# Kernel tuning notes

Measured on AMD Instinct MI355X. Metric: run time of the kernel, lower is better.

## Reference

```python
import jax, jax.numpy as jnp
import numpy as np

N_NODES = 250
IN_F = 18
OUT_F = 48
NEG_SLOPE = 0.2
EPS = 1e-16


def gat_conv(x, edge_index, w_gat, att_src, att_dst, b_gat):
    # PyG GATConv, heads=1, concat=True, add_self_loops=True
    n = x.shape[0]
    h = x @ w_gat.T                      # [N, OUT_F]
    loop = jnp.arange(n)
    src = jnp.concatenate([edge_index[0], loop])
    dst = jnp.concatenate([edge_index[1], loop])
    a_s = h @ att_src                    # [N]
    a_d = h @ att_dst                    # [N]
    e = jax.nn.leaky_relu(a_s[src] + a_d[dst], NEG_SLOPE)  # [E+N]
    m = jax.ops.segment_max(e, dst, num_segments=n)
    ex = jnp.exp(e - m[dst])
    denom = jax.ops.segment_sum(ex, dst, num_segments=n)
    alpha = ex / (denom[dst] + EPS)
    out = jax.ops.segment_sum(alpha[:, None] * h[src], dst, num_segments=n)
    return out + b_gat


def setup_inputs() -> dict:
    key = jax.random.key(0)
    ks = jax.random.split(key, 24)

    def lin(kw, kb, out_d, in_d):
        s = 1.0 / np.sqrt(in_d)
        W = jax.random.uniform(kw, (out_d, in_d), minval=-s, maxval=s, dtype=jnp.float32)
        b = jax.random.uniform(kb, (out_d,), minval=-s, maxval=s, dtype=jnp.float32)
        return W, b

    x = jax.random.normal(ks[0], (N_NODES, IN_F), dtype=jnp.float32)
    edge_index = jax.random.randint(ks[1], (2, 4000), 0, N_NODES)
    edge_weight = jax.random.uniform(ks[2], (4000,), dtype=jnp.float32)
    residue_onehot = jax.random.uniform(ks[3], (8,), dtype=jnp.float32)
    pssm = jax.random.normal(ks[4], (20,), dtype=jnp.float32)

    w_gat = jax.random.normal(ks[5], (OUT_F, IN_F), dtype=jnp.float32) * (1.0 / np.sqrt(IN_F))
    att_src = jax.random.normal(ks[6], (OUT_F,), dtype=jnp.float32) * 0.1
    att_dst = jax.random.normal(ks[7], (OUT_F,), dtype=jnp.float32) * 0.1
    b_gat = jnp.zeros((OUT_F,), dtype=jnp.float32)

    W0, b0 = lin(ks[8], ks[9], 4000, 12000)
    W1, b1 = lin(ks[10], ks[11], 800, 4028)
    W2, b2 = lin(ks[12], ks[13], 400, 800)
    W3, b3 = lin(ks[14], ks[15], 200, 400)
    W4, b4 = lin(ks[16], ks[17], 1, 200)

    return dict(x=x, edge_index=edge_index, edge_weight=edge_weight,
                residue_onehot=residue_onehot, pssm=pssm,
                w_gat=w_gat, att_src=att_src, att_dst=att_dst, b_gat=b_gat,
                W0=W0, b0=b0, W1=W1, b1=b1, W2=W2, b2=b2,
                W3=W3, b3=b3, W4=W4, b4=b4)


def reference(x, edge_index, edge_weight, residue_onehot, pssm,
              w_gat, att_src, att_dst, b_gat,
              W0, b0, W1, b1, W2, b2, W3, b3, W4, b4):
    # edge_weight is accepted but unused (matches original GAT.forward).
    h = jax.nn.relu(gat_conv(x, edge_index, w_gat, att_src, att_dst, b_gat))  # [250, 48]
    v = h.reshape(-1)                                   # [12000]
    v = jax.nn.relu(W0 @ v + b0)                        # [4000]
    v = jnp.concatenate([residue_onehot.reshape(-1), pssm, v])  # [4028]
    # Dropout in eval mode = identity
    v = jax.nn.relu(W1 @ v + b1)
    v = jax.nn.relu(W2 @ v + b2)
    v = jax.nn.relu(W3 @ v + b3)
    v = W4 @ v + b4                                     # [1]
    return v
```

## Files before the change

### kernel.cpp

```cpp
#include <hip/hip_runtime.h>

#define N_NODES 250
#define IN_F    18
#define OUT_F   48
#define E_EDGES 4000
#define E_TOT   (E_EDGES + N_NODES)

#define WS_H     0
#define WS_AS    12000
#define WS_AD    12250
#define WS_DEN   12500
#define WS_EX    12750
#define WS_VRAW  17000
#define WS_V1    29000
#define WS_V2    33028
#define WS_V2B   33828
#define WS_V3    34228

__global__ void k1_prep(const float* __restrict__ x, const float* __restrict__ wg,
                        const float* __restrict__ att_src, const float* __restrict__ att_dst,
                        const float* __restrict__ b_gat,
                        const float* __restrict__ roh, const float* __restrict__ pssm,
                        float* __restrict__ ws) {
    const int n = blockIdx.x;
    const int f = threadIdx.x;
    float hv = 0.f;
    if (f < OUT_F) {
        const float* xr = x + n * IN_F;
        const float* wr = wg + f * IN_F;
        #pragma unroll
        for (int k = 0; k < IN_F; ++k) hv += xr[k] * wr[k];
        ws[WS_H + n * OUT_F + f]    = hv;
        ws[WS_VRAW + n * OUT_F + f] = b_gat[f];
    }
    float cs = (f < OUT_F) ? hv * att_src[f] : 0.f;
    float cd = (f < OUT_F) ? hv * att_dst[f] : 0.f;
    #pragma unroll
    for (int o = 32; o > 0; o >>= 1) {
        cs += __shfl_down(cs, o);
        cd += __shfl_down(cd, o);
    }
    if (f == 0) {
        ws[WS_AS + n] = cs;
        ws[WS_AD + n] = cd;
        ws[WS_DEN + n] = 0.f;
    }
    if (n == 0 && f < 28) ws[WS_V1 + f] = (f < 8) ? roh[f] : pssm[f - 8];
}

__global__ void k2_edge(const int* __restrict__ ei, float* __restrict__ ws) {
    const int e = blockIdx.x * blockDim.x + threadIdx.x;
    if (e >= E_TOT) return;
    int s, d;
    if (e < E_EDGES) { s = ei[e]; d = ei[E_EDGES + e]; }
    else             { s = d = e - E_EDGES; }
    float val = ws[WS_AS + s] + ws[WS_AD + d];
    val = (val > 0.f) ? val : 0.2f * val;
    float ex = expf(val);
    atomicAdd(ws + WS_DEN + d, ex);
    ws[WS_EX + e] = ex;
}

__global__ void k3_accum(const int* __restrict__ ei, float* __restrict__ ws) {
    const int t = blockIdx.x * blockDim.x + threadIdx.x;
    const int e = t / OUT_F;
    const int f = t - e * OUT_F;
    if (e >= E_TOT) return;
    int s, d;
    if (e < E_EDGES) { s = ei[e]; d = ei[E_EDGES + e]; }
    else             { s = d = e - E_EDGES; }
    const float alpha = ws[WS_EX + e] / (ws[WS_DEN + d] + 1e-16f);
    atomicAdd(ws + WS_VRAW + d * OUT_F + f, alpha * ws[WS_H + s * OUT_F + f]);
}

template <int C, bool RELU_IN, bool RELU_OUT>
__global__ void matvec(const float* __restrict__ W, const float* __restrict__ b,
                       const float* __restrict__ vin, float* __restrict__ vout,
                       int rows) {
    const int wv   = threadIdx.x >> 6;
    const int lane = threadIdx.x & 63;
    const int row  = blockIdx.x * (blockDim.x >> 6) + wv;
    if (row >= rows) return;
    const float4* Wr = reinterpret_cast<const float4*>(W + (size_t)row * C);
    const float4* vi = reinterpret_cast<const float4*>(vin);
    constexpr int C4 = C / 4;
    float acc = 0.f;
    #pragma unroll 4
    for (int i = lane; i < C4; i += 64) {
        float4 w = Wr[i];
        float4 v = vi[i];
        if (RELU_IN) {
            v.x = fmaxf(v.x, 0.f); v.y = fmaxf(v.y, 0.f);
            v.z = fmaxf(v.z, 0.f); v.w = fmaxf(v.w, 0.f);
        }
        acc += w.x * v.x + w.y * v.y + w.z * v.z + w.w * v.w;
    }
    #pragma unroll
    for (int o = 32; o > 0; o >>= 1) acc += __shfl_down(acc, o);
    if (lane == 0) {
        float r = acc + b[row];
        vout[row] = RELU_OUT ? fmaxf(r, 0.f) : r;
    }
}

__global__ void k_w4(const float* __restrict__ W4, const float* __restrict__ b4,
                     const float* __restrict__ v3, float* __restrict__ out) {
    const int lane = threadIdx.x & 63;
    const float4* W4v = reinterpret_cast<const float4*>(W4);
    const float4* v3v = reinterpret_cast<const float4*>(v3);
    float acc = 0.f;
    for (int i = lane; i < 50; i += 64) {
        float4 w = W4v[i], v = v3v[i];
        acc += w.x * v.x + w.y * v.y + w.z * v.z + w.w * v.w;
    }
    #pragma unroll
    for (int o = 32; o > 0; o >>= 1) acc += __shfl_down(acc, o);
    if (lane == 0) out[0] = acc + b4[0];
}

extern "C" void kernel_launch(void* const* d_in, const int* in_sizes, int n_in,
                              void* d_out, int out_size, void* d_ws, size_t ws_size,
                              hipStream_t stream) {
    const float* x       = (const float*)d_in[0];
    const int*   ei      = (const int*)  d_in[1];
    const float* roh     = (const float*)d_in[3];
    const float* pssm    = (const float*)d_in[4];
    const float* wg      = (const float*)d_in[5];
    const float* att_src = (const float*)d_in[6];
    const float* att_dst = (const float*)d_in[7];
    const float* b_gat   = (const float*)d_in[8];
    const float* W0 = (const float*)d_in[9];   const float* b0 = (const float*)d_in[10];
    const float* W1 = (const float*)d_in[11];  const float* b1 = (const float*)d_in[12];
    const float* W2 = (const float*)d_in[13];  const float* b2 = (const float*)d_in[14];
    const float* W3 = (const float*)d_in[15];  const float* b3 = (const float*)d_in[16];
    const float* W4 = (const float*)d_in[17];  const float* b4 = (const float*)d_in[18];

    float* ws  = (float*)d_ws;
    float* out = (float*)d_out;

    k1_prep<<<N_NODES, 64, 0, stream>>>(x, wg, att_src, att_dst, b_gat, roh, pssm, ws);
    k2_edge<<<(E_TOT + 255) / 256, 256, 0, stream>>>(ei, ws);
    k3_accum<<<(E_TOT * OUT_F + 255) / 256, 256, 0, stream>>>(ei, ws);

    matvec<12000, true,  true><<<1000, 256, 0, stream>>>(W0, b0, ws + WS_VRAW, ws + WS_V1 + 28, 4000);
    matvec<4028,  false, true><<<200,  256, 0, stream>>>(W1, b1, ws + WS_V1, ws + WS_V2, 800);
    matvec<800,   false, true><<<100,  256, 0, stream>>>(W2, b2, ws + WS_V2, ws + WS_V2B, 400);
    matvec<400,   false, true><<<50,   256, 0, stream>>>(W3, b3, ws + WS_V2B, ws + WS_V3, 200);
    k_w4<<<1, 64, 0, stream>>>(W4, b4, ws + WS_V3, out);
}
```

Baseline: 330.0 us.

## Replace atomic scatter GAT aggregation with CSR build and per-node gather

The edge-softmax and aggregation stage no longer scatters with float atomics into global memory. A single block now builds a CSR grouping of edges by destination and computes the exp scores, then one block per node gathers its incoming edges and normalizes by the denominator locally. The matvec weight loads are also switched to nontemporal loads, since the large weight matrices are streamed only once. In exchange the CSR build is serial on one block with a single-thread prefix scan, which may add latency.

```diff
diff --git a/kernel.cpp b/kernel.cpp
--- a/kernel.cpp
+++ b/kernel.cpp
@@ -5,21 +5,24 @@
 #define OUT_F   48
 #define E_EDGES 4000
 #define E_TOT   (E_EDGES + N_NODES)
+#define EPS_F   1e-16f
+
+typedef float fx4 __attribute__((ext_vector_type(4)));
 
 #define WS_H     0
 #define WS_AS    12000
 #define WS_AD    12250
-#define WS_DEN   12500
-#define WS_EX    12750
-#define WS_VRAW  17000
-#define WS_V1    29000
-#define WS_V2    33028
-#define WS_V2B   33828
-#define WS_V3    34228
+#define WS_EX    12500
+#define WS_ROWP  16750
+#define WS_SLOT  17004
+#define WS_VRAW  21504
+#define WS_V1    33504
+#define WS_V2    37532
+#define WS_V2B   38332
+#define WS_V3    38732
 
 __global__ void k1_prep(const float* __restrict__ x, const float* __restrict__ wg,
                         const float* __restrict__ att_src, const float* __restrict__ att_dst,
-                        const float* __restrict__ b_gat,
                         const float* __restrict__ roh, const float* __restrict__ pssm,
                         float* __restrict__ ws) {
     const int n = blockIdx.x;
@@ -30,8 +33,7 @@
         const float* wr = wg + f * IN_F;
         #pragma unroll
         for (int k = 0; k < IN_F; ++k) hv += xr[k] * wr[k];
-        ws[WS_H + n * OUT_F + f]    = hv;
-        ws[WS_VRAW + n * OUT_F + f] = b_gat[f];
+        ws[WS_H + n * OUT_F + f] = hv;
     }
     float cs = (f < OUT_F) ? hv * att_src[f] : 0.f;
     float cd = (f < OUT_F) ? hv * att_dst[f] : 0.f;
@@ -43,34 +45,82 @@
     if (f == 0) {
         ws[WS_AS + n] = cs;
         ws[WS_AD + n] = cd;
-        ws[WS_DEN + n] = 0.f;
     }
     if (n == 0 && f < 28) ws[WS_V1 + f] = (f < 8) ? roh[f] : pssm[f - 8];
 }
 
-__global__ void k2_edge(const int* __restrict__ ei, float* __restrict__ ws) {
-    const int e = blockIdx.x * blockDim.x + threadIdx.x;
-    if (e >= E_TOT) return;
-    int s, d;
-    if (e < E_EDGES) { s = ei[e]; d = ei[E_EDGES + e]; }
-    else             { s = d = e - E_EDGES; }
-    float val = ws[WS_AS + s] + ws[WS_AD + d];
-    val = (val > 0.f) ? val : 0.2f * val;
-    float ex = expf(val);
-    atomicAdd(ws + WS_DEN + d, ex);
-    ws[WS_EX + e] = ex;
-}
-
-__global__ void k3_accum(const int* __restrict__ ei, float* __restrict__ ws) {
-    const int t = blockIdx.x * blockDim.x + threadIdx.x;
-    const int e = t / OUT_F;
-    const int f = t - e * OUT_F;
-    if (e >= E_TOT) return;
-    int s, d;
-    if (e < E_EDGES) { s = ei[e]; d = ei[E_EDGES + e]; }
-    else             { s = d = e - E_EDGES; }
-    const float alpha = ws[WS_EX + e] / (ws[WS_DEN + d] + 1e-16f);
-    atomicAdd(ws + WS_VRAW + d * OUT_F + f, alpha * ws[WS_H + s * OUT_F + f]);
+__global__ void k2_csr(const int* __restrict__ ei, float* __restrict__ ws) {
+    __shared__ int cnt[N_NODES];
+    __shared__ int rowp[N_NODES + 1];
+    __shared__ int pos[N_NODES];
+    const int tid = threadIdx.x;
+    const int nt  = blockDim.x;
+    for (int i = tid; i < N_NODES; i += nt) cnt[i] = 0;
+    __syncthreads();
+    const float* a_s = ws + WS_AS;
+    const float* a_d = ws + WS_AD;
+    float* ex = ws + WS_EX;
+    for (int e = tid; e < E_TOT; e += nt) {
+        int s, d;
+        if (e < E_EDGES) { s = ei[e]; d = ei[E_EDGES + e]; }
+        else             { s = d = e - E_EDGES; }
+        atomicAdd(&cnt[d], 1);
+        float val = a_s[s] + a_d[d];
+        val = (val > 0.f) ? val : 0.2f * val;
+        ex[e] = expf(val);
+    }
+    __syncthreads();
+    if (tid == 0) {
+        int run = 0;
+        for (int i = 0; i < N_NODES; ++i) { rowp[i] = run; run += cnt[i]; }
+        rowp[N_NODES] = run;
+    }
+    __syncthreads();
+    int* rowp_g = (int*)(ws + WS_ROWP);
+    for (int i = tid; i <= N_NODES; i += nt) { rowp_g[i] = rowp[i]; }
+    for (int i = tid; i < N_NODES; i += nt)  { pos[i] = rowp[i]; }
+    __syncthreads();
+    int* slots = (int*)(ws + WS_SLOT);
+    for (int e = tid; e < E_TOT; e += nt) {
+        int d;
+        if (e < E_EDGES) d = ei[E_EDGES + e];
+        else             d = e - E_EDGES;
+        int p = atomicAdd(&pos[d], 1);
+        slots[p] = e;
+    }
+}
+
+__global__ void k3_gather(const int* __restrict__ ei, const float* __restrict__ b_gat,
+                          float* __restrict__ ws) {
+    const int n = blockIdx.x;
+    const int t = threadIdx.x;
+    const int* rowp  = (const int*)(ws + WS_ROWP);
+    const int* slots = (const int*)(ws + WS_SLOT);
+    __shared__ int   s_src[64];
+    __shared__ float s_ex[64];
+    const int lo = rowp[n], hi = rowp[n + 1];
+    float acc = 0.f;
+    float den = 0.f;
+    for (int base = lo; base < hi; base += 64) {
+        const int m = min(64, hi - base);
+        if (t < m) {
+            int e = slots[base + t];
+            s_src[t] = (e < E_EDGES) ? ei[e] : e - E_EDGES;
+            s_ex[t]  = ws[WS_EX + e];
+        }
+        __syncthreads();
+        float dv = (t < m) ? s_ex[t] : 0.f;
+        #pragma unroll
+        for (int o = 32; o > 0; o >>= 1) dv += __shfl_down(dv, o);
+        den += __shfl(dv, 0);
+        if (t < OUT_F) {
+            for (int j = 0; j < m; ++j)
+                acc += s_ex[j] * ws[WS_H + s_src[j] * OUT_F + t];
+        }
+        __syncthreads();
+    }
+    if (t < OUT_F)
+        ws[WS_VRAW + n * OUT_F + t] = b_gat[t] + acc / (den + EPS_F);
 }
 
 template <int C, bool RELU_IN, bool RELU_OUT>
@@ -81,13 +131,13 @@
     const int lane = threadIdx.x & 63;
     const int row  = blockIdx.x * (blockDim.x >> 6) + wv;
     if (row >= rows) return;
-    const float4* Wr = reinterpret_cast<const float4*>(W + (size_t)row * C);
+    const fx4*    Wr = reinterpret_cast<const fx4*>(W + (size_t)row * C);
     const float4* vi = reinterpret_cast<const float4*>(vin);
     constexpr int C4 = C / 4;
     float acc = 0.f;
     #pragma unroll 4
     for (int i = lane; i < C4; i += 64) {
-        float4 w = Wr[i];
+        fx4    w = __builtin_nontemporal_load(&Wr[i]);
         float4 v = vi[i];
         if (RELU_IN) {
             v.x = fmaxf(v.x, 0.f); v.y = fmaxf(v.y, 0.f);
@@ -138,9 +188,9 @@
     float* ws  = (float*)d_ws;
     float* out = (float*)d_out;
 
-    k1_prep<<<N_NODES, 64, 0, stream>>>(x, wg, att_src, att_dst, b_gat, roh, pssm, ws);
-    k2_edge<<<(E_TOT + 255) / 256, 256, 0, stream>>>(ei, ws);
-    k3_accum<<<(E_TOT * OUT_F + 255) / 256, 256, 0, stream>>>(ei, ws);
+    k1_prep<<<N_NODES, 64, 0, stream>>>(x, wg, att_src, att_dst, roh, pssm, ws);
+    k2_csr<<<1, 1024, 0, stream>>>(ei, ws);
+    k3_gather<<<N_NODES, 64, 0, stream>>>(ei, b_gat, ws);
 
     matvec<12000, true,  true><<<1000, 256, 0, stream>>>(W0, b0, ws + WS_VRAW, ws + WS_V1 + 28, 4000);
     matvec<4028,  false, true><<<200,  256, 0, stream>>>(W1, b1, ws + WS_V1, ws + WS_V2, 800);
```

New measurement: 318.4 us. 1.04x faster.
